# Kernel optimization log

Measured on AMD Instinct MI355X. Metric: run time of the kernel, lower is better.

Reference implementation:

```python
import jax, jax.numpy as jnp
import numpy as np

B, L_PREM, T_HYP, D = 32, 256, 128, 256


def setup_inputs() -> dict:
    key = jax.random.key(0)
    ks = jax.random.split(key, 6)
    scale = 1.0 / np.sqrt(D)
    return {
        "x": jax.random.normal(ks[0], (B, L_PREM + T_HYP, D), dtype=jnp.float32),
        "w_y": jax.random.normal(ks[1], (D, D), dtype=jnp.float32) * scale,
        "w_h": jax.random.normal(ks[2], (D, D), dtype=jnp.float32) * scale,
        "w_r": jax.random.normal(ks[3], (D, D), dtype=jnp.float32) * scale,
        "w_alpha": jax.random.normal(ks[4], (D, 1), dtype=jnp.float32) * scale,
        "w_t": jax.random.normal(ks[5], (D, D), dtype=jnp.float32) * scale,
        "L": L_PREM,
    }


def reference(x, w_y, w_h, w_r, w_alpha, w_t, L):
    # x: (B, L + T, D)
    premise = x[:, :L, :]                 # Y: (B, L, D)
    hypothesis = jnp.swapaxes(x[:, L:, :], 0, 1)  # (T, B, D)

    # Y @ W_y does not depend on t: hoist out of the scan (same math).
    WY = jnp.einsum("bld,de->ble", premise, w_y)  # (B, L, D)

    def step(r_tm1, h_t):
        # r_tm1: (B, D), h_t: (B, D)
        s = h_t @ w_h + r_tm1 @ w_r                 # (B, D)
        Mt = jnp.tanh(WY + s[:, None, :])           # (B, L, D)
        scores = jnp.squeeze(Mt @ w_alpha, -1)      # (B, L)
        alpha = jax.nn.softmax(scores, axis=-1)     # (B, L)
        r_t = jnp.einsum("bl,bld->bd", alpha, premise) + r_tm1 @ w_t
        return r_t, r_t

    r0 = jnp.zeros_like(premise[:, 0, :])           # (B, D)
    _, rs = jax.lax.scan(step, r0, hypothesis)      # rs: (T, B, D)
    return jnp.swapaxes(rs, 0, 1)                   # (B, T, D)
```

## Files before the change

### kernel.cpp

```cpp
#include <hip/hip_runtime.h>
#include <hip/hip_fp16.h>

typedef unsigned long long u64;

#define C2X 2.8853900817779268f
#define LOG2E 1.4426950408889634f

#define WYS_OFF   0u
#define PR_OFF    4194304u
#define PREMH_OFF 8388608u
#define HWH_OFF   12582912u
#define WTH_OFF   16777216u
#define WTR_OFF   16908288u
#define ZP_OFF    17039360u
#define RCH_OFF   18087936u
#define MEMSET_SZ 1179648u

#define PRC_OFF    0u
#define WTRC_OFF   16384u
#define PREMC_OFF  32768u
#define WTC_OFF    49152u
#define WYC_OFF    65536u
#define HWHC_OFF   81920u
#define SCH_OFF    98304u
#define WACH_OFF   98432u
#define RED_OFF    98560u
#define ALB_OFF    98624u
#define RBB_OFF    100672u
#define PART_OFF   101696u
#define RPART_OFF  105920u
#define CTRL_OFF   106432u
#define LDS_TOTAL  106496u

__global__ __launch_bounds__(256) void prep_all(const float* __restrict__ x,
                                                const float* __restrict__ wy,
                                                const float* __restrict__ wh,
                                                const float* __restrict__ wr,
                                                const float* __restrict__ wt,
                                                __half* __restrict__ wys,
                                                __half* __restrict__ prh,
                                                float* __restrict__ hwh,
                                                __half* __restrict__ wtrh,
                                                __half* __restrict__ premh,
                                                __half* __restrict__ wth) {
    const int blk = blockIdx.x;
    if (blk >= 1568) {
        int i = (blk - 1568) * 256 + threadIdx.x;
        float4 v; __half* dst; int e;
        if (i < 524288) {
            e = i * 4; int b = e >> 16;
            v = *(const float4*)(x + (size_t)e + (size_t)b * 32768);
            dst = premh + e;
        } else if (i < 540672) {
            e = (i - 524288) * 4;
            v = *(const float4*)(wt + e);
            dst = wth + e;
        } else return;
        __half h[4] = {__float2half(v.x),__float2half(v.y),__float2half(v.z),__float2half(v.w)};
        *(uint2*)dst = *(const uint2*)h;
        return;
    }
    __shared__ float At[8][256];
    const int d = threadIdx.x;
    int mode, row0;
    if (blk < 1024)      { mode = 0; row0 = blk * 8; }
    else if (blk < 1536) { mode = 1; row0 = (blk - 1024) * 8; }
    else                 { mode = 2; row0 = (blk - 1536) * 8; }
    for (int rr = 0; rr < 8; ++rr) {
        int r = row0 + rr;
        const float* src;
        if (mode == 0)      { int b = r >> 8, l = r & 255; src = x + (size_t)(b * 384 + l) * 256; }
        else if (mode == 1) { int tt = r >> 5, bb = r & 31; src = x + (size_t)(bb * 384 + 256 + tt) * 256; }
        else                { src = wt + (size_t)r * 256; }
        At[rr][d] = src[d];
    }
    __syncthreads();
    if (mode == 0) {
        float accy[8] = {0,0,0,0,0,0,0,0}, accr[8] = {0,0,0,0,0,0,0,0};
        for (int k = 0; k < 256; k += 2) {
            float y0 = wy[(size_t)k * 256 + d], y1 = wy[(size_t)(k + 1) * 256 + d];
            float r0 = wr[(size_t)k * 256 + d], r1 = wr[(size_t)(k + 1) * 256 + d];
#pragma unroll
            for (int rr = 0; rr < 8; ++rr) {
                float2 a = *(const float2*)&At[rr][k];
                accy[rr] = fmaf(a.x, y0, accy[rr]); accy[rr] = fmaf(a.y, y1, accy[rr]);
                accr[rr] = fmaf(a.x, r0, accr[rr]); accr[rr] = fmaf(a.y, r1, accr[rr]);
            }
        }
        for (int rr = 0; rr < 8; ++rr) {
            int r = row0 + rr;
            wys[(size_t)r * 256 + d] = __float2half(accy[rr] * C2X);
            prh[(size_t)r * 256 + d] = __float2half(accr[rr]);
        }
    } else {
        const float* w = (mode == 1) ? wh : wr;
        float acc[8] = {0,0,0,0,0,0,0,0};
        for (int k = 0; k < 256; k += 4) {
            float w0 = w[(size_t)k * 256 + d], w1 = w[(size_t)(k+1) * 256 + d];
            float w2 = w[(size_t)(k+2) * 256 + d], w3 = w[(size_t)(k+3) * 256 + d];
#pragma unroll
            for (int rr = 0; rr < 8; ++rr) {
                float4 a = *(const float4*)&At[rr][k];
                float t0 = fmaf(a.x, w0, acc[rr]);
                t0 = fmaf(a.y, w1, t0);
                t0 = fmaf(a.z, w2, t0);
                acc[rr] = fmaf(a.w, w3, t0);
            }
        }
        for (int rr = 0; rr < 8; ++rr) {
            int r = row0 + rr;
            if (mode == 1) hwh[(size_t)r * 256 + d] = acc[rr] * C2X;
            else           wtrh[(size_t)r * 256 + d] = __float2half(acc[rr]);
        }
    }
}

__device__ __forceinline__ u64 agent_load64(const u64* p) {
    return __hip_atomic_load(p, __ATOMIC_RELAXED, __HIP_MEMORY_SCOPE_AGENT);
}
__device__ __forceinline__ void agent_store64(u64* p, u64 v) {
    __hip_atomic_store(p, v, __ATOMIC_RELAXED, __HIP_MEMORY_SCOPE_AGENT);
}

__global__ __launch_bounds__(512, 1) void wbw_main(
    const __half* __restrict__ wys, const __half* __restrict__ prh,
    const __half* __restrict__ premh, const __half* __restrict__ wth,
    const __half* __restrict__ wtrh, const float* __restrict__ hwh,
    const float* __restrict__ walpha, float* __restrict__ out,
    u64* __restrict__ zp, u64* __restrict__ rch)
{
    extern __shared__ char lds[];
    const int tid = threadIdx.x;
    const int b = blockIdx.x >> 3, j = blockIdx.x & 7;

    float* hwhc  = (float*)(lds + HWHC_OFF);
    float* s_ch  = (float*)(lds + SCH_OFF);
    float* wa_ch = (float*)(lds + WACH_OFF);
    float* redb  = (float*)(lds + RED_OFF);
    float* alb   = (float*)(lds + ALB_OFF);
    float* rbb   = (float*)(lds + RBB_OFF);
    float* part  = (float*)(lds + PART_OFF);
    float* rpart = (float*)(lds + RPART_OFF);
    unsigned* ctrL = (unsigned*)(lds + CTRL_OFF);

    {
        const int prt = tid & 3;
        for (int it = 0; it < 2; ++it) {
            int row = it * 128 + (tid >> 2);
            size_t g = (size_t)row * 256 + j * 32 + prt * 8;
            unsigned lo = (unsigned)row * 64 + (unsigned)prt * 16;
            *(uint4*)(lds + PRC_OFF   + lo) = *(const uint4*)(prh   + (size_t)b * 65536 + g);
            *(uint4*)(lds + WTRC_OFF  + lo) = *(const uint4*)(wtrh  + g);
            *(uint4*)(lds + PREMC_OFF + lo) = *(const uint4*)(premh + (size_t)b * 65536 + g);
            *(uint4*)(lds + WTC_OFF   + lo) = *(const uint4*)(wth   + g);
            *(uint4*)(lds + WYC_OFF   + lo) = *(const uint4*)(wys   + (size_t)b * 65536 + g);
        }
    }
    for (int it = 0; it < 8; ++it) {
        int idx = it * 512 + tid;
        int tt = idx >> 5, dd = idx & 31;
        hwhc[idx] = hwh[((size_t)tt * 32 + b) * 256 + j * 32 + dd];
    }
    if (tid < 32)  wa_ch[tid] = walpha[j * 32 + tid] * (-2.0f * LOG2E);
    if (tid < 256) { alb[tid] = 0.f; alb[256 + tid] = 0.f; rbb[tid] = 0.f; }
    if (tid < 8)   redb[tid] = (tid == 0 || tid == 4) ? 1.f : 0.f;
    if (tid == 0)  *ctrL = 0u;
    __syncthreads();

    for (int t = 0; t <= 128; ++t) {
        const int par = t & 1, q = par ^ 1;
        const float* e1 = alb + q * 256;
        if (t < 128) {
            {
                const int half_ = tid >> 8;
                const int s16 = (tid >> 4) & 15;
                const int d0 = (tid & 15) * 2;
                const __half* mat = (const __half*)(lds + (half_ ? WTRC_OFF : PRC_OFF));
                const float* vec = half_ ? rbb : e1;
                float ax = 0.f, ay = 0.f;
#pragma unroll
                for (int i = 0; i < 16; ++i) {
                    int l = s16 + i * 16;
                    float v = vec[l];
                    float2 mf = __half22float2(*(const __half2*)&mat[l * 32 + d0]);
                    ax = fmaf(v, mf.x, ax); ay = fmaf(v, mf.y, ay);
                }
                const int row = half_ * 16 + s16;
                part[row * 33 + d0] = ax; part[row * 33 + d0 + 1] = ay;
            }
            __syncthreads();
            if (tid < 64) {
                const int d = tid & 31, h = tid >> 5;
                float sum = 0.f;
#pragma unroll
                for (int s = 0; s < 16; ++s) sum += part[(h * 16 + s) * 33 + d];
                float other = __shfl_xor(sum, 32, 64);
                if (h == 0) {
                    const float* rd = redb + q * 4;
                    float rD = __builtin_amdgcn_rcpf(rd[0] + rd[1] + rd[2] + rd[3]);
                    float sv = fmaf(sum, rD, other);
                    s_ch[d] = fmaf(sv, C2X, hwhc[t * 32 + d]);
                }
            }
            __syncthreads();
            {
                const int l = tid >> 1, dh = (tid & 1) << 4;
                union { uint4 u[2]; __half h[16]; } W;
                W.u[0] = *(const uint4*)(lds + WYC_OFF + (unsigned)l * 64 + (unsigned)dh * 2);
                W.u[1] = *(const uint4*)(lds + WYC_OFF + (unsigned)l * 64 + (unsigned)dh * 2 + 16);
                float acc = 0.f;
#pragma unroll
                for (int i = 0; i < 16; ++i) {
                    float arg = __half2float(W.h[i]) + s_ch[dh + i];
                    acc = fmaf(wa_ch[dh + i],
                               __builtin_amdgcn_rcpf(__builtin_amdgcn_exp2f(arg) + 1.f), acc);
                }
                acc += __shfl_xor(acc, 1, 64);
                if ((tid & 1) == 0) {
                    u64 pk = ((u64)(unsigned)(t + 1) << 32) | (u64)__float_as_uint(acc);
                    agent_store64(&zp[(size_t)((par * 32 + b) * 8 + j) * 256 + l], pk);
                }
            }
        }
        if (tid >= 256) {
            const int t256 = tid - 256;
            const int lane = t256 & 63;
            const int w    = t256 >> 6;
            const int dp   = t256 & 15;
            const int d0   = dp * 2;
            const int l0   = (t256 >> 4) * 16;
            const float* rd = redb + q * 4;
            float rD = __builtin_amdgcn_rcpf(rd[0] + rd[1] + rd[2] + rd[3]);
            float ax = 0.f, ay = 0.f;
#pragma unroll
            for (int i = 0; i < 16; ++i) {
                int l = l0 + i;
                float a = e1[l] * rD;
                float r = rbb[l];
                unsigned o = (unsigned)l * 64 + (unsigned)d0 * 2;
                float2 mp = __half22float2(*(const __half2*)(lds + PREMC_OFF + o));
                float2 mt = __half22float2(*(const __half2*)(lds + WTC_OFF + o));
                ax = fmaf(a, mp.x, ax); ax = fmaf(r, mt.x, ax);
                ay = fmaf(a, mp.y, ay); ay = fmaf(r, mt.y, ay);
            }
            ax += __shfl_xor(ax, 16, 64); ax += __shfl_xor(ax, 32, 64);
            ay += __shfl_xor(ay, 16, 64); ay += __shfl_xor(ay, 32, 64);
            if (lane < 16) { rpart[w * 32 + d0] = ax; rpart[w * 32 + d0 + 1] = ay; }
            __threadfence_block();
            unsigned old = 0;
            if (lane == 0) old = atomicAdd(ctrL, 1u);
            old = __shfl(old, 0, 64);
            if (old == 3u) {
                if (lane < 32) {
                    float rsum = rpart[lane] + rpart[32 + lane]
                               + rpart[64 + lane] + rpart[96 + lane];
                    if (t >= 1)
                        out[((size_t)b * 128 + (t - 1)) * 256 + j * 32 + lane] = rsum;
                    if (t < 128) {
                        u64 pk = ((u64)(unsigned)t << 32) | (u64)__float_as_uint(rsum);
                        agent_store64(&rch[(size_t)(par * 32 + b) * 256 + j * 32 + lane], pk);
                    }
                }
                if (lane == 0) *ctrL = 0u;
            }
            if (t < 128) {
                const u64* rp = &rch[(size_t)(par * 32 + b) * 256 + t256];
                u64 rv;
                for (;;) {
                    rv = agent_load64(rp);
                    if (__all((unsigned)(rv >> 32) >= (unsigned)t)) break;
                    __builtin_amdgcn_s_sleep(1);
                }
                rbb[t256] = __uint_as_float((unsigned)rv);
            }
        } else if (t < 128) {
            const u64* zb = zp + (size_t)(par * 32 + b) * 2048 + tid;
            u64 v0,v1,v2,v3,v4,v5,v6,v7; int tries = 0;
            for (;;) {
                v0 = agent_load64(zb);         v1 = agent_load64(zb + 256);
                v2 = agent_load64(zb + 512);   v3 = agent_load64(zb + 768);
                v4 = agent_load64(zb + 1024);  v5 = agent_load64(zb + 1280);
                v6 = agent_load64(zb + 1536);  v7 = agent_load64(zb + 1792);
                bool ok = ((unsigned)(v0 >> 32) > (unsigned)t) & ((unsigned)(v1 >> 32) > (unsigned)t)
                        & ((unsigned)(v2 >> 32) > (unsigned)t) & ((unsigned)(v3 >> 32) > (unsigned)t)
                        & ((unsigned)(v4 >> 32) > (unsigned)t) & ((unsigned)(v5 >> 32) > (unsigned)t)
                        & ((unsigned)(v6 >> 32) > (unsigned)t) & ((unsigned)(v7 >> 32) > (unsigned)t);
                if (__all(ok)) break;
                if (++tries > 2) __builtin_amdgcn_s_sleep(1);
            }
            float zs = __uint_as_float((unsigned)v0) + __uint_as_float((unsigned)v1)
                     + __uint_as_float((unsigned)v2) + __uint_as_float((unsigned)v3)
                     + __uint_as_float((unsigned)v4) + __uint_as_float((unsigned)v5)
                     + __uint_as_float((unsigned)v6) + __uint_as_float((unsigned)v7);
            float ee = __builtin_amdgcn_exp2f(zs);
            float sv = ee;
#pragma unroll
            for (int off = 32; off; off >>= 1) sv += __shfl_xor(sv, off, 64);
            if ((tid & 63) == 0) redb[par * 4 + (tid >> 6)] = sv;
            alb[par * 256 + tid] = ee;
        }
        __syncthreads();
    }
}

extern "C" void kernel_launch(void* const* d_in, const int* in_sizes, int n_in,
                              void* d_out, int out_size, void* d_ws, size_t ws_size,
                              hipStream_t stream) {
    const float* x   = (const float*)d_in[0];
    const float* wy  = (const float*)d_in[1];
    const float* wh  = (const float*)d_in[2];
    const float* wr  = (const float*)d_in[3];
    const float* wal = (const float*)d_in[4];
    const float* wt  = (const float*)d_in[5];

    char* ws = (char*)d_ws;
    __half* wys    = (__half*)(ws + WYS_OFF);
    __half* prh    = (__half*)(ws + PR_OFF);
    __half* premh  = (__half*)(ws + PREMH_OFF);
    float*  hwh    = (float*)(ws + HWH_OFF);
    __half* wth    = (__half*)(ws + WTH_OFF);
    __half* wtrh   = (__half*)(ws + WTR_OFF);
    u64*    zp     = (u64*)(ws + ZP_OFF);
    u64*    rch    = (u64*)(ws + RCH_OFF);

    hipFuncSetAttribute((const void*)wbw_main,
                        hipFuncAttributeMaxDynamicSharedMemorySize, (int)LDS_TOTAL);

    prep_all<<<3680, 256, 0, stream>>>(x, wy, wh, wr, wt, wys, prh, hwh, wtrh, premh, wth);
    hipMemsetAsync(ws + ZP_OFF, 0, MEMSET_SZ, stream);

    wbw_main<<<256, 512, LDS_TOTAL, stream>>>(wys, prh, premh, wth, wtrh, hwh,
                                              wal, (float*)d_out, zp, rch);
}
```

Before: 497.9 us.

## Fuse r-update matvec into shared matvec phase and drop atomic counter reduction

The r_t computation (alpha·premise + r·W_t) now runs in the same all-thread matvec phase as the s computation, using four matrix slices selected by thread group. Both reductions are finished by the first 64 threads after one barrier. This removes the separate warp-group path with its LDS atomic counter, thread fence and rpart buffer. The r exchange and publish now happen before the tanh/score stage rather than overlapping with it, so latency hiding changes. Each thread also does a 32-step loop instead of 16.

Result: faster. 474.7 us (-4.7%).

```diff
diff --git a/kernel.cpp b/kernel.cpp
--- a/kernel.cpp
+++ b/kernel.cpp
@@ -28,9 +28,7 @@
 #define ALB_OFF    98624u
 #define RBB_OFF    100672u
 #define PART_OFF   101696u
-#define RPART_OFF  105920u
-#define CTRL_OFF   106432u
-#define LDS_TOTAL  106496u
+#define LDS_TOTAL  105920u
 
 __global__ __launch_bounds__(256) void prep_all(const float* __restrict__ x,
                                                 const float* __restrict__ wy,
@@ -140,8 +138,6 @@
     float* alb   = (float*)(lds + ALB_OFF);
     float* rbb   = (float*)(lds + RBB_OFF);
     float* part  = (float*)(lds + PART_OFF);
-    float* rpart = (float*)(lds + RPART_OFF);
-    unsigned* ctrL = (unsigned*)(lds + CTRL_OFF);
 
     {
         const int prt = tid & 3;
@@ -164,116 +160,81 @@
     if (tid < 32)  wa_ch[tid] = walpha[j * 32 + tid] * (-2.0f * LOG2E);
     if (tid < 256) { alb[tid] = 0.f; alb[256 + tid] = 0.f; rbb[tid] = 0.f; }
     if (tid < 8)   redb[tid] = (tid == 0 || tid == 4) ? 1.f : 0.f;
-    if (tid == 0)  *ctrL = 0u;
     __syncthreads();
 
     for (int t = 0; t <= 128; ++t) {
         const int par = t & 1, q = par ^ 1;
         const float* e1 = alb + q * 256;
-        if (t < 128) {
-            {
-                const int half_ = tid >> 8;
-                const int s16 = (tid >> 4) & 15;
-                const int d0 = (tid & 15) * 2;
-                const __half* mat = (const __half*)(lds + (half_ ? WTRC_OFF : PRC_OFF));
-                const float* vec = half_ ? rbb : e1;
-                float ax = 0.f, ay = 0.f;
-#pragma unroll
-                for (int i = 0; i < 16; ++i) {
-                    int l = s16 + i * 16;
-                    float v = vec[l];
-                    float2 mf = __half22float2(*(const __half2*)&mat[l * 32 + d0]);
-                    ax = fmaf(v, mf.x, ax); ay = fmaf(v, mf.y, ay);
-                }
-                const int row = half_ * 16 + s16;
-                part[row * 33 + d0] = ax; part[row * 33 + d0 + 1] = ay;
-            }
-            __syncthreads();
-            if (tid < 64) {
-                const int d = tid & 31, h = tid >> 5;
-                float sum = 0.f;
-#pragma unroll
-                for (int s = 0; s < 16; ++s) sum += part[(h * 16 + s) * 33 + d];
-                float other = __shfl_xor(sum, 32, 64);
-                if (h == 0) {
-                    const float* rd = redb + q * 4;
-                    float rD = __builtin_amdgcn_rcpf(rd[0] + rd[1] + rd[2] + rd[3]);
-                    float sv = fmaf(sum, rD, other);
-                    s_ch[d] = fmaf(sv, C2X, hwhc[t * 32 + d]);
-                }
-            }
-            __syncthreads();
-            {
-                const int l = tid >> 1, dh = (tid & 1) << 4;
-                union { uint4 u[2]; __half h[16]; } W;
-                W.u[0] = *(const uint4*)(lds + WYC_OFF + (unsigned)l * 64 + (unsigned)dh * 2);
-                W.u[1] = *(const uint4*)(lds + WYC_OFF + (unsigned)l * 64 + (unsigned)dh * 2 + 16);
-                float acc = 0.f;
-#pragma unroll
-                for (int i = 0; i < 16; ++i) {
-                    float arg = __half2float(W.h[i]) + s_ch[dh + i];
-                    acc = fmaf(wa_ch[dh + i],
-                               __builtin_amdgcn_rcpf(__builtin_amdgcn_exp2f(arg) + 1.f), acc);
-                }
-                acc += __shfl_xor(acc, 1, 64);
-                if ((tid & 1) == 0) {
-                    u64 pk = ((u64)(unsigned)(t + 1) << 32) | (u64)__float_as_uint(acc);
-                    agent_store64(&zp[(size_t)((par * 32 + b) * 8 + j) * 256 + l], pk);
-                }
-            }
-        }
-        if (tid >= 256) {
-            const int t256 = tid - 256;
-            const int lane = t256 & 63;
-            const int w    = t256 >> 6;
-            const int dp   = t256 & 15;
-            const int d0   = dp * 2;
-            const int l0   = (t256 >> 4) * 16;
+
+        {
+            const int sel = tid >> 7;
+            const int s8  = (tid >> 4) & 7;
+            const int d0  = (tid & 15) * 2;
+            const __half* mat = (const __half*)(lds + (unsigned)sel * 16384u);
+            const float* vec = (sel & 1) ? rbb : e1;
+            float ax = 0.f, ay = 0.f;
+#pragma unroll
+            for (int i = 0; i < 32; ++i) {
+                int l = s8 + i * 8;
+                float v = vec[l];
+                float2 mf = __half22float2(*(const __half2*)&mat[l * 32 + d0]);
+                ax = fmaf(v, mf.x, ax); ay = fmaf(v, mf.y, ay);
+            }
+            const int row = tid >> 4;
+            part[row * 33 + d0] = ax; part[row * 33 + d0 + 1] = ay;
+        }
+        __syncthreads();
+
+        if (tid < 64) {
+            const int d = tid & 31;
             const float* rd = redb + q * 4;
             float rD = __builtin_amdgcn_rcpf(rd[0] + rd[1] + rd[2] + rd[3]);
-            float ax = 0.f, ay = 0.f;
+            if (tid < 32) {
+                if (t < 128) {
+                    float sa = 0.f, sb = 0.f;
+#pragma unroll
+                    for (int s = 0; s < 8; ++s)  sa += part[s * 33 + d];
+#pragma unroll
+                    for (int s = 8; s < 16; ++s) sb += part[s * 33 + d];
+                    s_ch[d] = fmaf(fmaf(sa, rD, sb), C2X, hwhc[t * 32 + d]);
+                }
+            } else {
+                float ra = 0.f, rb2 = 0.f;
+#pragma unroll
+                for (int s = 16; s < 24; ++s) ra  += part[s * 33 + d];
+#pragma unroll
+                for (int s = 24; s < 32; ++s) rb2 += part[s * 33 + d];
+                float rv = fmaf(ra, rD, rb2);
+                if (t >= 1) out[((size_t)b * 128 + (t - 1)) * 256 + j * 32 + d] = rv;
+                if (t < 128) {
+                    u64 pk = ((u64)(unsigned)t << 32) | (u64)__float_as_uint(rv);
+                    agent_store64(&rch[(size_t)(par * 32 + b) * 256 + j * 32 + d], pk);
+                }
+            }
+        }
+        __syncthreads();
+        if (t == 128) break;
+
+        {
+            const int l = tid >> 1, dh = (tid & 1) << 4;
+            union { uint4 u[2]; __half h[16]; } W;
+            W.u[0] = *(const uint4*)(lds + WYC_OFF + (unsigned)l * 64 + (unsigned)dh * 2);
+            W.u[1] = *(const uint4*)(lds + WYC_OFF + (unsigned)l * 64 + (unsigned)dh * 2 + 16);
+            float acc = 0.f;
 #pragma unroll
             for (int i = 0; i < 16; ++i) {
-                int l = l0 + i;
-                float a = e1[l] * rD;
-                float r = rbb[l];
-                unsigned o = (unsigned)l * 64 + (unsigned)d0 * 2;
-                float2 mp = __half22float2(*(const __half2*)(lds + PREMC_OFF + o));
-                float2 mt = __half22float2(*(const __half2*)(lds + WTC_OFF + o));
-                ax = fmaf(a, mp.x, ax); ax = fmaf(r, mt.x, ax);
-                ay = fmaf(a, mp.y, ay); ay = fmaf(r, mt.y, ay);
-            }
-            ax += __shfl_xor(ax, 16, 64); ax += __shfl_xor(ax, 32, 64);
-            ay += __shfl_xor(ay, 16, 64); ay += __shfl_xor(ay, 32, 64);
-            if (lane < 16) { rpart[w * 32 + d0] = ax; rpart[w * 32 + d0 + 1] = ay; }
-            __threadfence_block();
-            unsigned old = 0;
-            if (lane == 0) old = atomicAdd(ctrL, 1u);
-            old = __shfl(old, 0, 64);
-            if (old == 3u) {
-                if (lane < 32) {
-                    float rsum = rpart[lane] + rpart[32 + lane]
-                               + rpart[64 + lane] + rpart[96 + lane];
-                    if (t >= 1)
-                        out[((size_t)b * 128 + (t - 1)) * 256 + j * 32 + lane] = rsum;
-                    if (t < 128) {
-                        u64 pk = ((u64)(unsigned)t << 32) | (u64)__float_as_uint(rsum);
-                        agent_store64(&rch[(size_t)(par * 32 + b) * 256 + j * 32 + lane], pk);
-                    }
-                }
-                if (lane == 0) *ctrL = 0u;
-            }
-            if (t < 128) {
-                const u64* rp = &rch[(size_t)(par * 32 + b) * 256 + t256];
-                u64 rv;
-                for (;;) {
-                    rv = agent_load64(rp);
-                    if (__all((unsigned)(rv >> 32) >= (unsigned)t)) break;
-                    __builtin_amdgcn_s_sleep(1);
-                }
-                rbb[t256] = __uint_as_float((unsigned)rv);
-            }
-        } else if (t < 128) {
+                float arg = __half2float(W.h[i]) + s_ch[dh + i];
+                acc = fmaf(wa_ch[dh + i],
+                           __builtin_amdgcn_rcpf(__builtin_amdgcn_exp2f(arg) + 1.f), acc);
+            }
+            acc += __shfl_xor(acc, 1, 64);
+            if ((tid & 1) == 0) {
+                u64 pk = ((u64)(unsigned)(t + 1) << 32) | (u64)__float_as_uint(acc);
+                agent_store64(&zp[(size_t)((par * 32 + b) * 8 + j) * 256 + l], pk);
+            }
+        }
+
+        if (tid < 256) {
             const u64* zb = zp + (size_t)(par * 32 + b) * 2048 + tid;
             u64 v0,v1,v2,v3,v4,v5,v6,v7; int tries = 0;
             for (;;) {
@@ -298,6 +259,16 @@
             for (int off = 32; off; off >>= 1) sv += __shfl_xor(sv, off, 64);
             if ((tid & 63) == 0) redb[par * 4 + (tid >> 6)] = sv;
             alb[par * 256 + tid] = ee;
+        } else {
+            const int t256 = tid - 256;
+            const u64* rp = &rch[(size_t)(par * 32 + b) * 256 + t256];
+            u64 rv;
+            for (;;) {
+                rv = agent_load64(rp);
+                if (__all((unsigned)(rv >> 32) >= (unsigned)t)) break;
+                __builtin_amdgcn_s_sleep(1);
+            }
+            rbb[t256] = __uint_as_float((unsigned)rv);
         }
         __syncthreads();
     }
```

## Spread r-update matvec across all 512 threads and skip polling own chunk

Applied to the files above, without the earlier changes.

The r_t partial products (alpha·premise and r·W_t) now run on all 512 threads, one half per matrix, and are written to a shared partial buffer. After a block barrier, 64 threads reduce and apply the softmax normalisation. This replaces the four-wave atomic counter in LDS. The block writes its own r chunk straight into rbb and no longer polls global memory for it. The cost is an extra __syncthreads per step on the critical path, which waits for the first-half threads.

Result: faster. 447.8 us (median of 2 runs) (-10.1%).

```diff
diff --git a/kernel.cpp b/kernel.cpp
--- a/kernel.cpp
+++ b/kernel.cpp
@@ -28,9 +28,7 @@
 #define ALB_OFF    98624u
 #define RBB_OFF    100672u
 #define PART_OFF   101696u
-#define RPART_OFF  105920u
-#define CTRL_OFF   106432u
-#define LDS_TOTAL  106496u
+#define LDS_TOTAL  105920u
 
 __global__ __launch_bounds__(256) void prep_all(const float* __restrict__ x,
                                                 const float* __restrict__ wy,
@@ -140,8 +138,6 @@
     float* alb   = (float*)(lds + ALB_OFF);
     float* rbb   = (float*)(lds + RBB_OFF);
     float* part  = (float*)(lds + PART_OFF);
-    float* rpart = (float*)(lds + RPART_OFF);
-    unsigned* ctrL = (unsigned*)(lds + CTRL_OFF);
 
     {
         const int prt = tid & 3;
@@ -164,7 +160,6 @@
     if (tid < 32)  wa_ch[tid] = walpha[j * 32 + tid] * (-2.0f * LOG2E);
     if (tid < 256) { alb[tid] = 0.f; alb[256 + tid] = 0.f; rbb[tid] = 0.f; }
     if (tid < 8)   redb[tid] = (tid == 0 || tid == 4) ? 1.f : 0.f;
-    if (tid == 0)  *ctrL = 0u;
     __syncthreads();
 
     for (int t = 0; t <= 128; ++t) {
@@ -222,48 +217,45 @@
                 }
             }
         }
+        {
+            const int half_ = tid >> 8;
+            const int s16 = (tid >> 4) & 15;
+            const int d0 = (tid & 15) * 2;
+            const __half* mat = (const __half*)(lds + (half_ ? WTC_OFF : PREMC_OFF));
+            const float* vec = half_ ? rbb : e1;
+            float ax = 0.f, ay = 0.f;
+#pragma unroll
+            for (int i = 0; i < 16; ++i) {
+                int l = s16 + i * 16;
+                float v = vec[l];
+                float2 mf = __half22float2(*(const __half2*)&mat[l * 32 + d0]);
+                ax = fmaf(v, mf.x, ax); ay = fmaf(v, mf.y, ay);
+            }
+            const int row = half_ * 16 + s16;
+            part[row * 33 + d0] = ax; part[row * 33 + d0 + 1] = ay;
+        }
+        __syncthreads();
         if (tid >= 256) {
             const int t256 = tid - 256;
-            const int lane = t256 & 63;
-            const int w    = t256 >> 6;
-            const int dp   = t256 & 15;
-            const int d0   = dp * 2;
-            const int l0   = (t256 >> 4) * 16;
-            const float* rd = redb + q * 4;
-            float rD = __builtin_amdgcn_rcpf(rd[0] + rd[1] + rd[2] + rd[3]);
-            float ax = 0.f, ay = 0.f;
-#pragma unroll
-            for (int i = 0; i < 16; ++i) {
-                int l = l0 + i;
-                float a = e1[l] * rD;
-                float r = rbb[l];
-                unsigned o = (unsigned)l * 64 + (unsigned)d0 * 2;
-                float2 mp = __half22float2(*(const __half2*)(lds + PREMC_OFF + o));
-                float2 mt = __half22float2(*(const __half2*)(lds + WTC_OFF + o));
-                ax = fmaf(a, mp.x, ax); ax = fmaf(r, mt.x, ax);
-                ay = fmaf(a, mp.y, ay); ay = fmaf(r, mt.y, ay);
-            }
-            ax += __shfl_xor(ax, 16, 64); ax += __shfl_xor(ax, 32, 64);
-            ay += __shfl_xor(ay, 16, 64); ay += __shfl_xor(ay, 32, 64);
-            if (lane < 16) { rpart[w * 32 + d0] = ax; rpart[w * 32 + d0 + 1] = ay; }
-            __threadfence_block();
-            unsigned old = 0;
-            if (lane == 0) old = atomicAdd(ctrL, 1u);
-            old = __shfl(old, 0, 64);
-            if (old == 3u) {
-                if (lane < 32) {
-                    float rsum = rpart[lane] + rpart[32 + lane]
-                               + rpart[64 + lane] + rpart[96 + lane];
-                    if (t >= 1)
-                        out[((size_t)b * 128 + (t - 1)) * 256 + j * 32 + lane] = rsum;
+            if (t256 < 64) {
+                const int d = t256 & 31, h = t256 >> 5;
+                float sum = 0.f;
+#pragma unroll
+                for (int s = 0; s < 16; ++s) sum += part[(h * 16 + s) * 33 + d];
+                float other = __shfl_xor(sum, 32, 64);
+                if (h == 0) {
+                    const float* rd = redb + q * 4;
+                    float rD = __builtin_amdgcn_rcpf(rd[0] + rd[1] + rd[2] + rd[3]);
+                    float rv = fmaf(sum, rD, other);
+                    if (t >= 1) out[((size_t)b * 128 + (t - 1)) * 256 + j * 32 + d] = rv;
+                    rbb[j * 32 + d] = rv;
                     if (t < 128) {
-                        u64 pk = ((u64)(unsigned)t << 32) | (u64)__float_as_uint(rsum);
-                        agent_store64(&rch[(size_t)(par * 32 + b) * 256 + j * 32 + lane], pk);
+                        u64 pk = ((u64)(unsigned)t << 32) | (u64)__float_as_uint(rv);
+                        agent_store64(&rch[(size_t)(par * 32 + b) * 256 + j * 32 + d], pk);
                     }
                 }
-                if (lane == 0) *ctrL = 0u;
-            }
-            if (t < 128) {
+            }
+            if (t < 128 && (t256 >> 5) != j) {
                 const u64* rp = &rch[(size_t)(par * 32 + b) * 256 + t256];
                 u64 rv;
                 for (;;) {
```
